# Kernel tuning notes

Measured on AMD Instinct MI355X. Metric: run time of the kernel, lower is better.

## Reference

```python
import jax, jax.numpy as jnp
import numpy as np

WIN = 7
NUM_HEADS = 4
DIM = 128
HEAD_DIM = DIM // NUM_HEADS
N = WIN * WIN
NW = 1024   # windows per image (224/7)^2
B_ = 16384  # batch(16) * NW


def _pos_index(win):
    # Swin relative-position index, static int table [N, N]
    coords = np.stack(np.meshgrid(np.arange(win), np.arange(win), indexing='ij'))
    cf = coords.reshape(2, -1)                       # [2, N]
    rel = cf[:, :, None] - cf[:, None, :]            # [2, N, N]
    rel = rel.transpose(1, 2, 0).astype(np.int64)    # [N, N, 2]
    rel[:, :, 0] += win - 1
    rel[:, :, 1] += win - 1
    rel[:, :, 0] *= 2 * win - 1
    return rel.sum(-1)                               # [N, N]

POS_INDEX = jnp.asarray(_pos_index(WIN))


def setup_inputs() -> dict:
    key = jax.random.key(0)
    ks = jax.random.split(key, 11)
    s = 0.02
    return {
        'x': jax.random.normal(ks[0], (B_, N, DIM), jnp.float32),
        'mask': jax.random.normal(ks[1], (NW, N, N), jnp.float32),
        'Wq': jax.random.normal(ks[2], (DIM, DIM), jnp.float32) * s,
        'bq': jax.random.normal(ks[3], (DIM,), jnp.float32) * s,
        'Wk': jax.random.normal(ks[4], (DIM, DIM), jnp.float32) * s,
        'bk': jax.random.normal(ks[5], (DIM,), jnp.float32) * s,
        'Wv': jax.random.normal(ks[6], (DIM, DIM), jnp.float32) * s,
        'bv': jax.random.normal(ks[7], (DIM,), jnp.float32) * s,
        'Wproj': jax.random.normal(ks[8], (DIM, DIM), jnp.float32) * s,
        'bproj': jax.random.normal(ks[9], (DIM,), jnp.float32) * s,
        'rel_bias': jax.random.normal(ks[10], ((2 * WIN - 1) ** 2, NUM_HEADS), jnp.float32) * s,
    }


def reference(x, mask, Wq, bq, Wk, bk, Wv, bv, Wproj, bproj, rel_bias):
    Bw, n, C = x.shape
    H, hd = NUM_HEADS, HEAD_DIM
    scale = hd ** -0.5

    def heads(t):  # [B, N, C] -> [B, H, N, hd]
        return t.reshape(Bw, n, H, hd).transpose(0, 2, 1, 3)

    q = heads(x @ Wq.T + bq) * scale
    k = heads(x @ Wk.T + bk)
    v = heads(x @ Wv.T + bv)

    attn = jnp.einsum('bhnd,bhmd->bhnm', q, k)              # [B, H, N, N]
    rb = rel_bias[POS_INDEX.reshape(-1)].reshape(n, n, H)    # [N, N, H]
    attn = attn + rb.transpose(2, 0, 1)[None]                # + [1, H, N, N]

    nw = mask.shape[0]
    attn = attn.reshape(Bw // nw, nw, H, n, n) + mask[None, :, None]
    attn = attn.reshape(Bw, H, n, n)

    attn = jax.nn.softmax(attn, axis=-1)
    out = jnp.einsum('bhnm,bhmd->bhnd', attn, v)             # [B, H, N, hd]
    out = out.transpose(0, 2, 1, 3).reshape(Bw, n, C)
    return out @ Wproj.T + bproj
```

## Files before the change

### kernel.cpp

```cpp
#include <hip/hip_runtime.h>
#include <hip/hip_bf16.h>
#include <stdint.h>

#define NTOK 49
#define LOG2E 1.4426950408889634f
#define SCALE2 0.25507662683243807f

typedef __attribute__((ext_vector_type(4))) float f32x4;
typedef __attribute__((ext_vector_type(2))) unsigned int u32x2;
typedef __attribute__((ext_vector_type(4))) unsigned int u32x4;
typedef __attribute__((ext_vector_type(8))) short bfrag;
typedef __attribute__((ext_vector_type(4))) short s16x4;
typedef __attribute__((ext_vector_type(4))) float facc;

#define MFMA16(A,B,C) __builtin_amdgcn_mfma_f32_16x16x32_bf16(A,B,C,0,0,0)
#define EXP2(x) __builtin_amdgcn_exp2f(x)

__device__ __forceinline__ unsigned pk2bf(float a, float b) {
    unsigned r;
    asm("v_cvt_pk_bf16_f32 %0, %1, %2" : "=v"(r) : "v"(a), "v"(b));
    return r;
}
__device__ __forceinline__ short f2bf(float a) {
    unsigned ua = __builtin_bit_cast(unsigned, a);
    ua = ua + 0x7fffu + ((ua >> 16) & 1u);
    return (short)(ua >> 16);
}
__device__ __forceinline__ float bf2f(short s) {
    unsigned u = ((unsigned)(unsigned short)s) << 16;
    return __builtin_bit_cast(float, u);
}
__device__ __forceinline__ int sw256(int row, int cb) { return row * 256 + (cb ^ ((row & 7) << 4)); }
__device__ __forceinline__ int sw128(int row, int cb) { return row * 128 + (cb ^ ((row & 7) << 4)); }

__global__ void prep_w(const float* __restrict__ Wq, const float* __restrict__ Wk,
                       const float* __restrict__ Wv, const float* __restrict__ Wp,
                       const float* __restrict__ relb, short* __restrict__ ws)
{
    int t = blockIdx.x * 256 + threadIdx.x;
    if (t >= 16384) return;
    int e = t & 7, lane = (t >> 3) & 63, ks = (t >> 9) & 3, tile = t >> 11;
    int row = tile * 16 + (lane & 15);
    int col = ks * 32 + (lane >> 4) * 8 + e;
    int src = row * 128 + col;
    ws[t]         = f2bf(Wq[src]);
    ws[16384 + t] = f2bf(Wk[src]);
    ws[32768 + t] = f2bf(Wv[src]);
    ws[49152 + t] = f2bf(Wp[src]);
    int e2 = t & 3, lane2 = (t >> 2) & 63, mt = (t >> 8) & 3, rt = (t >> 10) & 3, h = t >> 12;
    int r = rt * 16 + (lane2 & 15);
    int m = mt * 16 + (lane2 >> 4) * 4 + e2;
    float v = 0.f;
    if (r < NTOK && m < NTOK) {
        int idx = ((r / 7 - m / 7) + 6) * 13 + ((r % 7) - (m % 7) + 6);
        v = relb[idx * 4 + h] * LOG2E;
    }
    ws[65536 + t] = f2bf(v);
}

__global__ void prep_cmb(const float* __restrict__ mask, const float* __restrict__ relb,
                         short* __restrict__ cmb)
{
    int t = blockIdx.x * 256 + threadIdx.x;
    int e = t & 3, lane = (t >> 2) & 63, mt = (t >> 8) & 3, rt = (t >> 10) & 3;
    int h = (t >> 12) & 3, w = t >> 14;
    int r = rt * 16 + (lane & 15);
    int m = mt * 16 + (lane >> 4) * 4 + e;
    float v = -1e30f;
    if (r < NTOK && m < NTOK) {
        int idx = ((r / 7 - m / 7) + 6) * 13 + ((r % 7) - (m % 7) + 6);
        v = (mask[w * (NTOK * NTOK) + r * NTOK + m] + relb[idx * 4 + h]) * LOG2E;
    }
    cmb[t] = f2bf(v);
}

__device__ __forceinline__ char* pstrip(char* smem_, int wid, int r, int mb) {
    return smem_ + ((mb >> 6) << 14) + r * 256 + ((wid * 64 + (mb & 63)) ^ ((r & 7) << 4));
}

template<bool CMBF>
__global__ __launch_bounds__(256, 2) void swin_fwd(
    const float* __restrict__ x, const float* __restrict__ mask,
    const float* __restrict__ bq, const float* __restrict__ bk,
    const float* __restrict__ bv, const float* __restrict__ bp,
    const short* __restrict__ wqf, const short* __restrict__ wkf,
    const short* __restrict__ wvf, const short* __restrict__ wpf,
    const short* __restrict__ rbf, const short* __restrict__ cmbf,
    float* __restrict__ out)
{
    extern __shared__ char smem[];
    char* qbuf  = smem;
    char* kbuf  = smem + 16384;
    char* vtbuf = smem + 32768;
    char* r4    = smem + 49152;

    const int win = blockIdx.x;
    const int tid = threadIdx.x;
    const int wid = tid >> 6;
    const int lane = tid & 63;
    const int l16 = lane & 15;
    const int lg = lane >> 4;

    {
        const float* xw = x + (size_t)win * (NTOK * 128);
        #pragma unroll
        for (int i = 0; i < 7; ++i) {
            int i4 = i * 256 + tid;
            if (i4 < 1568) {
                f32x4 f = *(const f32x4*)(xw + i4 * 4);
                int tok = i4 >> 5, col = (i4 & 31) * 4;
                u32x2 w; w.x = pk2bf(f.x, f.y); w.y = pk2bf(f.z, f.w);
                *(u32x2*)(r4 + sw256(tok, col * 2)) = w;
            }
        }
        if (tid < 240) {
            u32x4 z = {0, 0, 0, 0};
            *(u32x4*)(r4 + 49 * 256 + tid * 16) = z;
        }
    }
    bfrag aq[2][4], ak[2][4], av[2][4];
    float bqv[2][4], bkv[2][4], bvv2[2];
    #pragma unroll
    for (int mt = 0; mt < 2; ++mt) {
        #pragma unroll
        for (int ks = 0; ks < 4; ++ks) {
            int fi = (((wid * 2 + mt) * 4 + ks) * 64 + lane) * 8;
            aq[mt][ks] = *(const bfrag*)(wqf + fi);
            ak[mt][ks] = *(const bfrag*)(wkf + fi);
            av[mt][ks] = *(const bfrag*)(wvf + fi);
        }
        #pragma unroll
        for (int j = 0; j < 4; ++j) {
            int o = wid * 32 + mt * 16 + lg * 4 + j;
            bqv[mt][j] = bq[o]; bkv[mt][j] = bk[o];
        }
        bvv2[mt] = bv[wid * 32 + mt * 16 + l16];
    }
    __syncthreads();

    {
        #pragma unroll
        for (int nt = 0; nt < 4; ++nt) {
            bfrag bx[4];
            #pragma unroll
            for (int ks = 0; ks < 4; ++ks)
                bx[ks] = *(const bfrag*)(r4 + sw256(nt * 16 + l16, (ks * 32 + lg * 8) * 2));
            facc accq[2] = {{0,0,0,0},{0,0,0,0}};
            facc acck[2] = {{0,0,0,0},{0,0,0,0}};
            facc accv[2] = {{0,0,0,0},{0,0,0,0}};
            #pragma unroll
            for (int ks = 0; ks < 4; ++ks)
                #pragma unroll
                for (int mt = 0; mt < 2; ++mt) {
                    accq[mt] = MFMA16(aq[mt][ks], bx[ks], accq[mt]);
                    acck[mt] = MFMA16(ak[mt][ks], bx[ks], acck[mt]);
                    accv[mt] = MFMA16(bx[ks], av[mt][ks], accv[mt]);
                }
            int tok = nt * 16 + l16;
            #pragma unroll
            for (int mt = 0; mt < 2; ++mt) {
                int o0 = wid * 32 + mt * 16 + lg * 4;
                u32x2 wq2, wk2, wv2;
                wq2.x = pk2bf((accq[mt][0] + bqv[mt][0]) * SCALE2, (accq[mt][1] + bqv[mt][1]) * SCALE2);
                wq2.y = pk2bf((accq[mt][2] + bqv[mt][2]) * SCALE2, (accq[mt][3] + bqv[mt][3]) * SCALE2);
                wk2.x = pk2bf(acck[mt][0] + bkv[mt][0], acck[mt][1] + bkv[mt][1]);
                wk2.y = pk2bf(acck[mt][2] + bkv[mt][2], acck[mt][3] + bkv[mt][3]);
                *(u32x2*)(qbuf + sw256(tok, o0 * 2)) = wq2;
                *(u32x2*)(kbuf + sw256(tok, o0 * 2)) = wk2;
                wv2.x = pk2bf(accv[mt][0] + bvv2[mt], accv[mt][1] + bvv2[mt]);
                wv2.y = pk2bf(accv[mt][2] + bvv2[mt], accv[mt][3] + bvv2[mt]);
                *(u32x2*)(vtbuf + sw128(wid * 32 + mt * 16 + l16, (nt * 16 + lg * 4) * 2)) = wv2;
            }
        }
    }

    facc s[4][4];
    {
        bfrag ka[4], qb[4];
        int cb = (wid * 32 + lg * 8) * 2;
        #pragma unroll
        for (int t = 0; t < 4; ++t) {
            ka[t] = *(const bfrag*)(kbuf + sw256(t * 16 + l16, cb));
            qb[t] = *(const bfrag*)(qbuf + sw256(t * 16 + l16, cb));
        }
        #pragma unroll
        for (int mt = 0; mt < 4; ++mt)
            #pragma unroll
            for (int rt = 0; rt < 4; ++rt) {
                facc z = {0, 0, 0, 0};
                s[mt][rt] = MFMA16(ka[mt], qb[rt], z);
            }
    }

    s16x4 b4r[4][4];
    if (CMBF) {
        const short* cw = cmbf + ((size_t)(win & 1023) * 4 + wid) * 4096;
        #pragma unroll
        for (int rt = 0; rt < 4; ++rt)
            #pragma unroll
            for (int mt = 0; mt < 4; ++mt)
                b4r[rt][mt] = *(const s16x4*)(cw + (rt * 4 + mt) * 256 + lane * 4);
    }

    if (CMBF) {
        __syncthreads();
    } else {
        __syncthreads();
        const float* mw = mask + (size_t)(win & 1023) * (NTOK * NTOK);
        #pragma unroll
        for (int i = 0; i < 16; ++i) {
            int flat = i * 256 + tid;
            int r = flat >> 6, m = flat & 63;
            float v = -1e30f;
            if (r < NTOK && m < NTOK) v = mw[r * 49 + m] * LOG2E;
            *(float*)(r4 + sw256(r, m * 4)) = v;
        }
        __syncthreads();
    }

    float rs4[4];
    {
        #pragma unroll
        for (int rt = 0; rt < 4; ++rt) {
            int r = rt * 16 + l16;
            float lgt[4][4];
            float mx = -3e38f;
            #pragma unroll
            for (int mt = 0; mt < 4; ++mt) {
                if (CMBF) {
                    #pragma unroll
                    for (int j = 0; j < 4; ++j) {
                        float v = s[mt][rt][j] + bf2f(b4r[rt][mt][j]);
                        lgt[mt][j] = v;
                        mx = fmaxf(mx, v);
                    }
                } else {
                    s16x4 b4 = *(const s16x4*)(rbf + ((wid * 16 + rt * 4 + mt) * 64 + lane) * 4);
                    f32x4 mk = *(const f32x4*)(r4 + sw256(r, (mt * 16 + lg * 4) * 4));
                    #pragma unroll
                    for (int j = 0; j < 4; ++j) {
                        float v = s[mt][rt][j] + bf2f(b4[j]) + mk[j];
                        lgt[mt][j] = v;
                        mx = fmaxf(mx, v);
                    }
                }
            }
            mx = fmaxf(mx, __shfl_xor(mx, 16));
            mx = fmaxf(mx, __shfl_xor(mx, 32));
            float sum = 0.f;
            u32x2 pw[4];
            #pragma unroll
            for (int mt = 0; mt < 4; ++mt) {
                float p0 = EXP2(lgt[mt][0] - mx);
                float p1 = EXP2(lgt[mt][1] - mx);
                float p2 = EXP2(lgt[mt][2] - mx);
                float p3 = EXP2(lgt[mt][3] - mx);
                sum += (p0 + p1) + (p2 + p3);
                pw[mt].x = pk2bf(p0, p1);
                pw[mt].y = pk2bf(p2, p3);
            }
            sum += __shfl_xor(sum, 16);
            sum += __shfl_xor(sum, 32);
            rs4[rt] = __builtin_amdgcn_rcpf(sum);
            #pragma unroll
            for (int mt = 0; mt < 4; ++mt)
                *(u32x2*)pstrip(smem, wid, r, mt * 32 + lg * 8) = pw[mt];
        }
    }

    facc o2[2][4];
    {
        #pragma unroll
        for (int ct = 0; ct < 2; ++ct)
            #pragma unroll
            for (int rt = 0; rt < 4; ++rt) o2[ct][rt] = (facc){0, 0, 0, 0};
        #pragma unroll
        for (int ks = 0; ks < 2; ++ks) {
            bfrag avf[2], pb[4];
            #pragma unroll
            for (int ct = 0; ct < 2; ++ct)
                avf[ct] = *(const bfrag*)(vtbuf + sw128(wid * 32 + ct * 16 + l16, (ks * 32 + lg * 8) * 2));
            #pragma unroll
            for (int rt = 0; rt < 4; ++rt)
                pb[rt] = *(const bfrag*)pstrip(smem, wid, rt * 16 + l16, ks * 64 + lg * 16);
            #pragma unroll
            for (int ct = 0; ct < 2; ++ct)
                #pragma unroll
                for (int rt = 0; rt < 4; ++rt)
                    o2[ct][rt] = MFMA16(avf[ct], pb[rt], o2[ct][rt]);
        }
    }
    bfrag ap[2][4];
    float bpv[2][4];
    #pragma unroll
    for (int mt = 0; mt < 2; ++mt) {
        #pragma unroll
        for (int ks = 0; ks < 4; ++ks)
            ap[mt][ks] = *(const bfrag*)(wpf + (((wid * 2 + mt) * 4 + ks) * 64 + lane) * 8);
        #pragma unroll
        for (int j = 0; j < 4; ++j)
            bpv[mt][j] = bp[wid * 32 + mt * 16 + lg * 4 + j];
    }
    __syncthreads();
    {
        #pragma unroll
        for (int ct = 0; ct < 2; ++ct) {
            int c0 = wid * 32 + ct * 16 + lg * 4;
            #pragma unroll
            for (int rt = 0; rt < 4; ++rt) {
                int r = rt * 16 + l16;
                float sc = rs4[rt];
                u32x2 w;
                w.x = pk2bf(o2[ct][rt][0] * sc, o2[ct][rt][1] * sc);
                w.y = pk2bf(o2[ct][rt][2] * sc, o2[ct][rt][3] * sc);
                *(u32x2*)(r4 + sw256(r, c0 * 2)) = w;
            }
        }
    }
    __syncthreads();

    {
        facc acco[2][4];
        #pragma unroll
        for (int mt = 0; mt < 2; ++mt)
            #pragma unroll
            for (int tt = 0; tt < 4; ++tt) acco[mt][tt] = (facc){0, 0, 0, 0};
        #pragma unroll
        for (int tt = 0; tt < 4; ++tt) {
            bfrag ba[4];
            #pragma unroll
            for (int ks = 0; ks < 4; ++ks)
                ba[ks] = *(const bfrag*)(r4 + sw256(tt * 16 + l16, (ks * 32 + lg * 8) * 2));
            #pragma unroll
            for (int ks = 0; ks < 4; ++ks)
                #pragma unroll
                for (int mt = 0; mt < 2; ++mt)
                    acco[mt][tt] = MFMA16(ap[mt][ks], ba[ks], acco[mt][tt]);
        }
        float* ow = out + (size_t)win * (NTOK * 128);
        #pragma unroll
        for (int tt = 0; tt < 4; ++tt) {
            int tok = tt * 16 + l16;
            if (tok < NTOK) {
                #pragma unroll
                for (int mt = 0; mt < 2; ++mt) {
                    int o0 = wid * 32 + mt * 16 + lg * 4;
                    f32x4 w;
                    w.x = acco[mt][tt][0] + bpv[mt][0];
                    w.y = acco[mt][tt][1] + bpv[mt][1];
                    w.z = acco[mt][tt][2] + bpv[mt][2];
                    w.w = acco[mt][tt][3] + bpv[mt][3];
                    *(f32x4*)(ow + tok * 128 + o0) = w;
                }
            }
        }
    }
}

extern "C" void kernel_launch(void* const* d_in, const int* in_sizes, int n_in,
                              void* d_out, int out_size, void* d_ws, size_t ws_size,
                              hipStream_t stream)
{
    const float* x    = (const float*)d_in[0];
    const float* mask = (const float*)d_in[1];
    const float* Wq   = (const float*)d_in[2];
    const float* bq   = (const float*)d_in[3];
    const float* Wk   = (const float*)d_in[4];
    const float* bk   = (const float*)d_in[5];
    const float* Wv   = (const float*)d_in[6];
    const float* bv   = (const float*)d_in[7];
    const float* Wp   = (const float*)d_in[8];
    const float* bp   = (const float*)d_in[9];
    const float* rlb  = (const float*)d_in[10];
    short* ws = (short*)d_ws;
    short* cmb = ws + 81920;
    const size_t need = ((size_t)81920 + (size_t)16777216) * 2;
    const bool use_cmb = ws_size >= need;

    prep_w<<<64, 256, 0, stream>>>(Wq, Wk, Wv, Wp, rlb, ws);
    if (use_cmb) {
        prep_cmb<<<65536, 256, 0, stream>>>(mask, rlb, cmb);
        swin_fwd<true><<<16384, 256, 65536, stream>>>(x, mask, bq, bk, bv, bp,
            ws, ws + 16384, ws + 32768, ws + 49152, ws + 65536, cmb, (float*)d_out);
    } else {
        swin_fwd<false><<<16384, 256, 65536, stream>>>(x, mask, bq, bk, bv, bp,
            ws, ws + 16384, ws + 32768, ws + 49152, ws + 65536, cmb, (float*)d_out);
    }
}
```

Before: 406.2 us.

## Make Swin attention kernel persistent with register prefetch of next window

Replaces the one-block-per-window launch with a persistent kernel of 512 blocks, each looping over 32 windows. The next window's x tile is loaded into registers while the current window is computed, and is written to LDS after the QK step. MFMA sections are wrapped in s_setprio raises. The projection output is staged through qbuf so r4 can take the prefetched x. Weights are reloaded each iteration to limit register pressure, but 512 blocks may underfill the GPU and the extra live registers risk spills.

```diff
diff --git a/kernel.cpp b/kernel.cpp
--- a/kernel.cpp
+++ b/kernel.cpp
@@ -78,15 +78,13 @@
     return smem_ + ((mb >> 6) << 14) + r * 256 + ((wid * 64 + (mb & 63)) ^ ((r & 7) << 4));
 }
 
-template<bool CMBF>
-__global__ __launch_bounds__(256, 2) void swin_fwd(
-    const float* __restrict__ x, const float* __restrict__ mask,
+__global__ __launch_bounds__(256, 2) void swin_fwd_p(
+    const float* __restrict__ x,
     const float* __restrict__ bq, const float* __restrict__ bk,
     const float* __restrict__ bv, const float* __restrict__ bp,
     const short* __restrict__ wqf, const short* __restrict__ wkf,
     const short* __restrict__ wvf, const short* __restrict__ wpf,
-    const short* __restrict__ rbf, const short* __restrict__ cmbf,
-    float* __restrict__ out)
+    const short* __restrict__ cmbf, float* __restrict__ out)
 {
     extern __shared__ char smem[];
     char* qbuf  = smem;
@@ -94,6 +92,307 @@
     char* vtbuf = smem + 32768;
     char* r4    = smem + 49152;
 
+    const int b = blockIdx.x;
+    const int tid = threadIdx.x;
+    const int wid = tid >> 6;
+    const int lane = tid & 63;
+    const int l16 = lane & 15;
+    const int lg = lane >> 4;
+
+    float bqv[2][4], bkv[2][4], bpv[2][4], bvv2[2];
+    #pragma unroll
+    for (int mt = 0; mt < 2; ++mt) {
+        #pragma unroll
+        for (int j = 0; j < 4; ++j) {
+            int o = wid * 32 + mt * 16 + lg * 4 + j;
+            bqv[mt][j] = bq[o]; bkv[mt][j] = bk[o]; bpv[mt][j] = bp[o];
+        }
+        bvv2[mt] = bv[wid * 32 + mt * 16 + l16];
+    }
+
+    bfrag aq[2][4], ak[2][4], av[2][4];
+    {
+        const short* wq_i = wqf; const short* wk_i = wkf; const short* wv_i = wvf;
+        asm volatile("" : "+s"(wq_i), "+s"(wk_i), "+s"(wv_i));
+        #pragma unroll
+        for (int mt = 0; mt < 2; ++mt)
+            #pragma unroll
+            for (int ks = 0; ks < 4; ++ks) {
+                int fi = (((wid * 2 + mt) * 4 + ks) * 64 + lane) * 8;
+                aq[mt][ks] = *(const bfrag*)(wq_i + fi);
+                ak[mt][ks] = *(const bfrag*)(wk_i + fi);
+                av[mt][ks] = *(const bfrag*)(wv_i + fi);
+            }
+    }
+
+    f32x4 xr[7];
+    {
+        const float* xw0 = x + (size_t)b * 6272;
+        #pragma unroll
+        for (int ii = 0; ii < 7; ++ii) {
+            int i4 = ii * 256 + tid;
+            if (i4 < 1568) xr[ii] = *(const f32x4*)(xw0 + i4 * 4);
+        }
+        #pragma unroll
+        for (int ii = 0; ii < 7; ++ii) {
+            int i4 = ii * 256 + tid;
+            if (i4 < 1568) {
+                int tok = i4 >> 5, col = (i4 & 31) * 4;
+                u32x2 w; w.x = pk2bf(xr[ii].x, xr[ii].y); w.y = pk2bf(xr[ii].z, xr[ii].w);
+                *(u32x2*)(r4 + sw256(tok, col * 2)) = w;
+            }
+        }
+        if (tid < 240) { u32x4 z = {0, 0, 0, 0}; *(u32x4*)(r4 + 49 * 256 + tid * 16) = z; }
+    }
+    __syncthreads();
+
+    #pragma unroll 1
+    for (int it = 0; it < 32; ++it) {
+        const int win = b + (it << 9);
+
+        {
+            const float* xn = x + (size_t)((win + 512) & 16383) * 6272;
+            #pragma unroll
+            for (int ii = 0; ii < 7; ++ii) {
+                int i4 = ii * 256 + tid;
+                if (i4 < 1568) xr[ii] = *(const f32x4*)(xn + i4 * 4);
+            }
+        }
+
+        {
+            #pragma unroll
+            for (int nt = 0; nt < 4; ++nt) {
+                bfrag bx[4];
+                #pragma unroll
+                for (int ks = 0; ks < 4; ++ks)
+                    bx[ks] = *(const bfrag*)(r4 + sw256(nt * 16 + l16, (ks * 32 + lg * 8) * 2));
+                facc accq[2] = {{0,0,0,0},{0,0,0,0}};
+                facc acck[2] = {{0,0,0,0},{0,0,0,0}};
+                facc accv[2] = {{0,0,0,0},{0,0,0,0}};
+                __builtin_amdgcn_s_setprio(1);
+                #pragma unroll
+                for (int ks = 0; ks < 4; ++ks)
+                    #pragma unroll
+                    for (int mt = 0; mt < 2; ++mt) {
+                        accq[mt] = MFMA16(aq[mt][ks], bx[ks], accq[mt]);
+                        acck[mt] = MFMA16(ak[mt][ks], bx[ks], acck[mt]);
+                        accv[mt] = MFMA16(bx[ks], av[mt][ks], accv[mt]);
+                    }
+                __builtin_amdgcn_s_setprio(0);
+                int tok = nt * 16 + l16;
+                #pragma unroll
+                for (int mt = 0; mt < 2; ++mt) {
+                    int o0 = wid * 32 + mt * 16 + lg * 4;
+                    u32x2 wq2, wk2, wv2;
+                    wq2.x = pk2bf((accq[mt][0] + bqv[mt][0]) * SCALE2, (accq[mt][1] + bqv[mt][1]) * SCALE2);
+                    wq2.y = pk2bf((accq[mt][2] + bqv[mt][2]) * SCALE2, (accq[mt][3] + bqv[mt][3]) * SCALE2);
+                    wk2.x = pk2bf(acck[mt][0] + bkv[mt][0], acck[mt][1] + bkv[mt][1]);
+                    wk2.y = pk2bf(acck[mt][2] + bkv[mt][2], acck[mt][3] + bkv[mt][3]);
+                    *(u32x2*)(qbuf + sw256(tok, o0 * 2)) = wq2;
+                    *(u32x2*)(kbuf + sw256(tok, o0 * 2)) = wk2;
+                    wv2.x = pk2bf(accv[mt][0] + bvv2[mt], accv[mt][1] + bvv2[mt]);
+                    wv2.y = pk2bf(accv[mt][2] + bvv2[mt], accv[mt][3] + bvv2[mt]);
+                    *(u32x2*)(vtbuf + sw128(wid * 32 + mt * 16 + l16, (nt * 16 + lg * 4) * 2)) = wv2;
+                }
+            }
+        }
+
+        facc s[4][4];
+        {
+            bfrag ka[4], qb[4];
+            int cb = (wid * 32 + lg * 8) * 2;
+            #pragma unroll
+            for (int t = 0; t < 4; ++t) {
+                ka[t] = *(const bfrag*)(kbuf + sw256(t * 16 + l16, cb));
+                qb[t] = *(const bfrag*)(qbuf + sw256(t * 16 + l16, cb));
+            }
+            __builtin_amdgcn_s_setprio(1);
+            #pragma unroll
+            for (int mt = 0; mt < 4; ++mt)
+                #pragma unroll
+                for (int rt = 0; rt < 4; ++rt) {
+                    facc z = {0, 0, 0, 0};
+                    s[mt][rt] = MFMA16(ka[mt], qb[rt], z);
+                }
+            __builtin_amdgcn_s_setprio(0);
+        }
+        __syncthreads();
+
+        {
+            #pragma unroll
+            for (int ii = 0; ii < 7; ++ii) {
+                int i4 = ii * 256 + tid;
+                if (i4 < 1568) {
+                    int tok = i4 >> 5, col = (i4 & 31) * 4;
+                    u32x2 w; w.x = pk2bf(xr[ii].x, xr[ii].y); w.y = pk2bf(xr[ii].z, xr[ii].w);
+                    *(u32x2*)(r4 + sw256(tok, col * 2)) = w;
+                }
+            }
+        }
+
+        float rs4[4];
+        {
+            const short* cw = cmbf + ((size_t)((win & 1023) * 4 + wid) << 12);
+            #pragma unroll
+            for (int rt = 0; rt < 4; ++rt) {
+                float lgt[4][4];
+                float mx = -3e38f;
+                #pragma unroll
+                for (int mt = 0; mt < 4; ++mt) {
+                    s16x4 b4 = *(const s16x4*)(cw + ((rt * 4 + mt) << 8) + lane * 4);
+                    #pragma unroll
+                    for (int j = 0; j < 4; ++j) {
+                        float v = s[mt][rt][j] + bf2f(b4[j]);
+                        lgt[mt][j] = v;
+                        mx = fmaxf(mx, v);
+                    }
+                }
+                mx = fmaxf(mx, __shfl_xor(mx, 16));
+                mx = fmaxf(mx, __shfl_xor(mx, 32));
+                float sum = 0.f;
+                u32x2 pw[4];
+                #pragma unroll
+                for (int mt = 0; mt < 4; ++mt) {
+                    float p0 = EXP2(lgt[mt][0] - mx);
+                    float p1 = EXP2(lgt[mt][1] - mx);
+                    float p2 = EXP2(lgt[mt][2] - mx);
+                    float p3 = EXP2(lgt[mt][3] - mx);
+                    sum += (p0 + p1) + (p2 + p3);
+                    pw[mt].x = pk2bf(p0, p1);
+                    pw[mt].y = pk2bf(p2, p3);
+                }
+                sum += __shfl_xor(sum, 16);
+                sum += __shfl_xor(sum, 32);
+                rs4[rt] = __builtin_amdgcn_rcpf(sum);
+                int r = rt * 16 + l16;
+                #pragma unroll
+                for (int mt = 0; mt < 4; ++mt)
+                    *(u32x2*)pstrip(smem, wid, r, mt * 32 + lg * 8) = pw[mt];
+            }
+        }
+
+        facc o2[2][4];
+        {
+            #pragma unroll
+            for (int ct = 0; ct < 2; ++ct)
+                #pragma unroll
+                for (int rt = 0; rt < 4; ++rt) o2[ct][rt] = (facc){0, 0, 0, 0};
+            #pragma unroll
+            for (int ks = 0; ks < 2; ++ks) {
+                bfrag avf[2], pb[4];
+                #pragma unroll
+                for (int ct = 0; ct < 2; ++ct)
+                    avf[ct] = *(const bfrag*)(vtbuf + sw128(wid * 32 + ct * 16 + l16, (ks * 32 + lg * 8) * 2));
+                #pragma unroll
+                for (int rt = 0; rt < 4; ++rt)
+                    pb[rt] = *(const bfrag*)pstrip(smem, wid, rt * 16 + l16, ks * 64 + lg * 16);
+                __builtin_amdgcn_s_setprio(1);
+                #pragma unroll
+                for (int ct = 0; ct < 2; ++ct)
+                    #pragma unroll
+                    for (int rt = 0; rt < 4; ++rt)
+                        o2[ct][rt] = MFMA16(avf[ct], pb[rt], o2[ct][rt]);
+                __builtin_amdgcn_s_setprio(0);
+            }
+        }
+        bfrag ap[2][4];
+        {
+            const short* wp_i = wpf;
+            asm volatile("" : "+s"(wp_i));
+            #pragma unroll
+            for (int mt = 0; mt < 2; ++mt)
+                #pragma unroll
+                for (int ks = 0; ks < 4; ++ks)
+                    ap[mt][ks] = *(const bfrag*)(wp_i + (((wid * 2 + mt) * 4 + ks) * 64 + lane) * 8);
+        }
+        __syncthreads();
+        {
+            #pragma unroll
+            for (int ct = 0; ct < 2; ++ct) {
+                int c0 = wid * 32 + ct * 16 + lg * 4;
+                #pragma unroll
+                for (int rt = 0; rt < 4; ++rt) {
+                    int r = rt * 16 + l16;
+                    float sc = rs4[rt];
+                    u32x2 w;
+                    w.x = pk2bf(o2[ct][rt][0] * sc, o2[ct][rt][1] * sc);
+                    w.y = pk2bf(o2[ct][rt][2] * sc, o2[ct][rt][3] * sc);
+                    *(u32x2*)(qbuf + sw256(r, c0 * 2)) = w;
+                }
+            }
+        }
+        __syncthreads();
+
+        {
+            facc acco[2][4];
+            #pragma unroll
+            for (int mt = 0; mt < 2; ++mt)
+                #pragma unroll
+                for (int tt = 0; tt < 4; ++tt) acco[mt][tt] = (facc){0, 0, 0, 0};
+            #pragma unroll
+            for (int tt = 0; tt < 4; ++tt) {
+                bfrag ba[4];
+                #pragma unroll
+                for (int ks = 0; ks < 4; ++ks)
+                    ba[ks] = *(const bfrag*)(qbuf + sw256(tt * 16 + l16, (ks * 32 + lg * 8) * 2));
+                __builtin_amdgcn_s_setprio(1);
+                #pragma unroll
+                for (int ks = 0; ks < 4; ++ks)
+                    #pragma unroll
+                    for (int mt = 0; mt < 2; ++mt)
+                        acco[mt][tt] = MFMA16(ap[mt][ks], ba[ks], acco[mt][tt]);
+                __builtin_amdgcn_s_setprio(0);
+            }
+            float* ow = out + (size_t)win * 6272;
+            #pragma unroll
+            for (int tt = 0; tt < 4; ++tt) {
+                int tok = tt * 16 + l16;
+                if (tok < NTOK) {
+                    #pragma unroll
+                    for (int mt = 0; mt < 2; ++mt) {
+                        int o0 = wid * 32 + mt * 16 + lg * 4;
+                        f32x4 w;
+                        w.x = acco[mt][tt][0] + bpv[mt][0];
+                        w.y = acco[mt][tt][1] + bpv[mt][1];
+                        w.z = acco[mt][tt][2] + bpv[mt][2];
+                        w.w = acco[mt][tt][3] + bpv[mt][3];
+                        *(f32x4*)(ow + tok * 128 + o0) = w;
+                    }
+                }
+            }
+        }
+
+        {
+            const short* wq_i = wqf; const short* wk_i = wkf; const short* wv_i = wvf;
+            asm volatile("" : "+s"(wq_i), "+s"(wk_i), "+s"(wv_i));
+            #pragma unroll
+            for (int mt = 0; mt < 2; ++mt)
+                #pragma unroll
+                for (int ks = 0; ks < 4; ++ks) {
+                    int fi = (((wid * 2 + mt) * 4 + ks) * 64 + lane) * 8;
+                    aq[mt][ks] = *(const bfrag*)(wq_i + fi);
+                    ak[mt][ks] = *(const bfrag*)(wk_i + fi);
+                    av[mt][ks] = *(const bfrag*)(wv_i + fi);
+                }
+        }
+        __syncthreads();
+    }
+}
+
+__global__ __launch_bounds__(256, 2) void swin_fwd_fb(
+    const float* __restrict__ x, const float* __restrict__ mask,
+    const float* __restrict__ bq, const float* __restrict__ bk,
+    const float* __restrict__ bv, const float* __restrict__ bp,
+    const short* __restrict__ wqf, const short* __restrict__ wkf,
+    const short* __restrict__ wvf, const short* __restrict__ wpf,
+    const short* __restrict__ rbf, float* __restrict__ out)
+{
+    extern __shared__ char smem[];
+    char* qbuf  = smem;
+    char* kbuf  = smem + 16384;
+    char* vtbuf = smem + 32768;
+    char* r4    = smem + 49152;
+
     const int win = blockIdx.x;
     const int tid = threadIdx.x;
     const int wid = tid >> 6;
@@ -102,7 +401,7 @@
     const int lg = lane >> 4;
 
     {
-        const float* xw = x + (size_t)win * (NTOK * 128);
+        const float* xw = x + (size_t)win * 6272;
         #pragma unroll
         for (int i = 0; i < 7; ++i) {
             int i4 = i * 256 + tid;
@@ -113,10 +412,7 @@
                 *(u32x2*)(r4 + sw256(tok, col * 2)) = w;
             }
         }
-        if (tid < 240) {
-            u32x4 z = {0, 0, 0, 0};
-            *(u32x4*)(r4 + 49 * 256 + tid * 16) = z;
-        }
+        if (tid < 240) { u32x4 z = {0, 0, 0, 0}; *(u32x4*)(r4 + 49 * 256 + tid * 16) = z; }
     }
     bfrag aq[2][4], ak[2][4], av[2][4];
     float bqv[2][4], bkv[2][4], bvv2[2];
@@ -173,7 +469,6 @@
             }
         }
     }
-
     facc s[4][4];
     {
         bfrag ka[4], qb[4];
@@ -191,21 +486,8 @@
                 s[mt][rt] = MFMA16(ka[mt], qb[rt], z);
             }
     }
-
-    s16x4 b4r[4][4];
-    if (CMBF) {
-        const short* cw = cmbf + ((size_t)(win & 1023) * 4 + wid) * 4096;
-        #pragma unroll
-        for (int rt = 0; rt < 4; ++rt)
-            #pragma unroll
-            for (int mt = 0; mt < 4; ++mt)
-                b4r[rt][mt] = *(const s16x4*)(cw + (rt * 4 + mt) * 256 + lane * 4);
-    }
-
-    if (CMBF) {
-        __syncthreads();
-    } else {
-        __syncthreads();
+    __syncthreads();
+    {
         const float* mw = mask + (size_t)(win & 1023) * (NTOK * NTOK);
         #pragma unroll
         for (int i = 0; i < 16; ++i) {
@@ -215,9 +497,8 @@
             if (r < NTOK && m < NTOK) v = mw[r * 49 + m] * LOG2E;
             *(float*)(r4 + sw256(r, m * 4)) = v;
         }
-        __syncthreads();
-    }
-
+    }
+    __syncthreads();
     float rs4[4];
     {
         #pragma unroll
@@ -227,22 +508,13 @@
             float mx = -3e38f;
             #pragma unroll
             for (int mt = 0; mt < 4; ++mt) {
-                if (CMBF) {
-                    #pragma unroll
-                    for (int j = 0; j < 4; ++j) {
-                        float v = s[mt][rt][j] + bf2f(b4r[rt][mt][j]);
-                        lgt[mt][j] = v;
-                        mx = fmaxf(mx, v);
-                    }
-                } else {
-                    s16x4 b4 = *(const s16x4*)(rbf + ((wid * 16 + rt * 4 + mt) * 64 + lane) * 4);
-                    f32x4 mk = *(const f32x4*)(r4 + sw256(r, (mt * 16 + lg * 4) * 4));
-                    #pragma unroll
-                    for (int j = 0; j < 4; ++j) {
-                        float v = s[mt][rt][j] + bf2f(b4[j]) + mk[j];
-                        lgt[mt][j] = v;
-                        mx = fmaxf(mx, v);
-                    }
+                s16x4 b4 = *(const s16x4*)(rbf + ((wid * 16 + rt * 4 + mt) * 64 + lane) * 4);
+                f32x4 mk = *(const f32x4*)(r4 + sw256(r, (mt * 16 + lg * 4) * 4));
+                #pragma unroll
+                for (int j = 0; j < 4; ++j) {
+                    float v = s[mt][rt][j] + bf2f(b4[j]) + mk[j];
+                    lgt[mt][j] = v;
+                    mx = fmaxf(mx, v);
                 }
             }
             mx = fmaxf(mx, __shfl_xor(mx, 16));
@@ -267,7 +539,6 @@
                 *(u32x2*)pstrip(smem, wid, r, mt * 32 + lg * 8) = pw[mt];
         }
     }
-
     facc o2[2][4];
     {
         #pragma unroll
@@ -318,7 +589,6 @@
         }
     }
     __syncthreads();
-
     {
         facc acco[2][4];
         #pragma unroll
@@ -337,7 +607,7 @@
                 for (int mt = 0; mt < 2; ++mt)
                     acco[mt][tt] = MFMA16(ap[mt][ks], ba[ks], acco[mt][tt]);
         }
-        float* ow = out + (size_t)win * (NTOK * 128);
+        float* ow = out + (size_t)win * 6272;
         #pragma unroll
         for (int tt = 0; tt < 4; ++tt) {
             int tok = tt * 16 + l16;
@@ -380,10 +650,10 @@
     prep_w<<<64, 256, 0, stream>>>(Wq, Wk, Wv, Wp, rlb, ws);
     if (use_cmb) {
         prep_cmb<<<65536, 256, 0, stream>>>(mask, rlb, cmb);
-        swin_fwd<true><<<16384, 256, 65536, stream>>>(x, mask, bq, bk, bv, bp,
-            ws, ws + 16384, ws + 32768, ws + 49152, ws + 65536, cmb, (float*)d_out);
+        swin_fwd_p<<<512, 256, 65536, stream>>>(x, bq, bk, bv, bp,
+            ws, ws + 16384, ws + 32768, ws + 49152, cmb, (float*)d_out);
     } else {
-        swin_fwd<false><<<16384, 256, 65536, stream>>>(x, mask, bq, bk, bv, bp,
-            ws, ws + 16384, ws + 32768, ws + 49152, ws + 65536, cmb, (float*)d_out);
-    }
-}
+        swin_fwd_fb<<<16384, 256, 65536, stream>>>(x, mask, bq, bk, bv, bp,
+            ws, ws + 16384, ws + 32768, ws + 49152, ws + 65536, (float*)d_out);
+    }
+}
```

New measurement: 370.6 us. 8.8% less time.
